# Kernel tuning notes

Hardware: AMD Instinct MI355X
Metric: run time of the kernel (lower is better)

Reference implementation:

```python
import jax, jax.numpy as jnp
import numpy as np
from jax import lax

B, T, IN, H, OUT, OC = 64, 1024, 128, 512, 128, 64


def setup_inputs() -> dict:
    key = jax.random.key(0)
    ks = jax.random.split(key, 9)
    s = 0.05
    return {
        "inX": jax.random.normal(ks[0], (B, T, IN), jnp.float32),
        "r": jnp.zeros((1,), jnp.float32),
        "conv_w": jax.random.normal(ks[1], (OC, IN, 3), jnp.float32) * s,
        "conv_b": jax.random.normal(ks[2], (OC,), jnp.float32) * s,
        "w_ih": jax.random.normal(ks[3], (4 * H, OC), jnp.float32) * s,
        "w_hh": jax.random.normal(ks[4], (4 * H, H), jnp.float32) * s,
        "b_ih": jax.random.normal(ks[5], (4 * H,), jnp.float32) * s,
        "b_hh": jax.random.normal(ks[6], (4 * H,), jnp.float32) * s,
        "lin_w": jax.random.normal(ks[7], (OUT, H), jnp.float32) * s,
        "lin_b": jax.random.normal(ks[8], (OUT,), jnp.float32) * s,
        "batch_size": B,
    }


def reference(inX, r, conv_w, conv_b, w_ih, w_hh, b_ih, b_hh, lin_w, lin_b, batch_size):
    # F.normalize along dim=2 (L2, eps=1e-12)
    nrm = jnp.sqrt(jnp.sum(inX * inX, axis=2, keepdims=True))
    x = inX / jnp.maximum(nrm, 1e-12)
    # [B, C, L] conv1d, valid padding, stride 1
    x = x.transpose(0, 2, 1)
    y = lax.conv_general_dilated(x, conv_w, (1,), "VALID",
                                 dimension_numbers=("NCH", "OIH", "NCH"))
    y = jax.nn.relu(y + conv_b[None, :, None])
    seq = y.transpose(2, 0, 1)  # [T', B, OC]

    h0 = jnp.zeros((batch_size, w_hh.shape[1]), inX.dtype)
    c0 = jnp.zeros_like(h0)

    def step(carry, xt):
        h, c = carry
        gates = xt @ w_ih.T + b_ih + h @ w_hh.T + b_hh
        i, f, g, o = jnp.split(gates, 4, axis=-1)
        c = jax.nn.sigmoid(f) * c + jax.nn.sigmoid(i) * jnp.tanh(g)
        h = jax.nn.sigmoid(o) * jnp.tanh(c)
        return (h, c), None

    (h, c), _ = lax.scan(step, (h0, c0), seq)
    return h @ lin_w.T + lin_b
```

## Files before the change

### kernel.cpp

```cpp
#include <hip/hip_runtime.h>

typedef __attribute__((ext_vector_type(8))) short short8;
typedef __attribute__((ext_vector_type(4))) float f32x4;
typedef unsigned short u16;
typedef unsigned long long u64;

#define TP   1022
#define NWRK 32

#define OFF_WPACK   0
#define OFF_SEQ     2359296
#define OFF_BIAS    10993664
#define OFF_H0      11001856
#define OFF_H1      11067392
#define OFF_HFIN    11132928
#define OFF_BAR     11264000
#define OFF_CWT     11266048

__device__ inline u16 f2bf(float x) {
  union { float f; unsigned u; } un; un.f = x;
  unsigned r = un.u + 0x7fffu + ((un.u >> 16) & 1u);
  return (u16)(r >> 16);
}
__device__ inline float sigmoidf_(float x) { return 1.f / (1.f + __expf(-x)); }
__device__ inline float tanhf_(float x)    { return 2.f / (1.f + __expf(-2.f * x)) - 1.f; }

__device__ inline f32x4 load16_sc0(const void* p) {
  f32x4 r;
  asm volatile("global_load_dwordx4 %0, %1, off sc0" : "=v"(r) : "v"(p) : "memory");
  return r;
}
__device__ inline void store16_sc0(void* p, f32x4 v) {
  asm volatile("global_store_dwordx4 %0, %1, off sc0" :: "v"(p), "v"(v) : "memory");
}

__global__ void k_init(const float* __restrict__ b_ih, const float* __restrict__ b_hh,
                       float* __restrict__ biasp, unsigned* __restrict__ hzero,
                       unsigned* __restrict__ bar) {
  int tid = blockIdx.x * 256 + threadIdx.x;
  if (tid < 32768) hzero[tid] = 0u;
  if (tid < 2048) {
    int j = tid >> 2, g = tid & 3;
    int row = g * 512 + j;
    biasp[tid] = b_ih[row] + b_hh[row];
  }
  if (tid < 128) bar[tid] = 0u;
}

__global__ void k_pack(const float* __restrict__ w_ih, const float* __restrict__ w_hh,
                       u16* __restrict__ wp) {
  int idx = blockIdx.x * 256 + threadIdx.x;
  int nt = idx / 9216;
  int rem = idx - nt * 9216;
  int kt = rem / 512;
  int rem2 = rem - kt * 512;
  int lane = rem2 >> 3, i = rem2 & 7;
  int n = nt * 16 + (lane & 15);
  int k = kt * 32 + (lane >> 4) * 8 + i;
  int j = n >> 2, g = n & 3;
  int row = g * 512 + j;
  float v = (k < 64) ? w_ih[row * 64 + k] : w_hh[row * 512 + (k - 64)];
  wp[idx] = f2bf(v);
}

__global__ void k_packc(const float* __restrict__ conv_w, float* __restrict__ cwT) {
  int idx = blockIdx.x * 256 + threadIdx.x;
  if (idx < 24576) {
    int ik = idx >> 6, oc = idx & 63;
    cwT[ik * 64 + oc] = conv_w[oc * 384 + ik];
  }
}

__global__ __launch_bounds__(256) void k_conv(const float* __restrict__ inX,
                                              const float* __restrict__ cwT,
                                              const float* __restrict__ conv_b,
                                              u16* __restrict__ seq) {
  __shared__ float xn[6][128];
  __shared__ float rn[6];
  int b = blockIdx.y;
  int t0 = blockIdx.x * 4;
  int tid = threadIdx.x;
  for (int e = tid; e < 768; e += 256) {
    int ri = e >> 7, col = e & 127;
    int t = t0 + ri;
    xn[ri][col] = (t < 1024) ? inX[((size_t)b * 1024 + t) * 128 + col] : 0.f;
  }
  __syncthreads();
  if (tid < 192) {
    int ri = tid >> 5, l32 = tid & 31;
    float4 v = *reinterpret_cast<const float4*>(&xn[ri][l32 * 4]);
    float s = v.x * v.x + v.y * v.y + v.z * v.z + v.w * v.w;
    #pragma unroll
    for (int d = 1; d < 32; d <<= 1) s += __shfl_xor(s, d, 32);
    if (l32 == 0) rn[ri] = 1.f / fmaxf(sqrtf(s), 1e-12f);
  }
  __syncthreads();
  for (int e = tid; e < 768; e += 256) {
    int ri = e >> 7, col = e & 127;
    xn[ri][col] *= rn[ri];
  }
  __syncthreads();
  int oc = tid & 63, ty = tid >> 6;
  int t = t0 + ty;
  if (t < TP) {
    const float* wt = cwT + oc;
    float s = conv_b[oc];
    #pragma unroll 8
    for (int i = 0; i < 128; ++i) {
      s += wt[(i * 3 + 0) * 64] * xn[ty + 0][i]
         + wt[(i * 3 + 1) * 64] * xn[ty + 1][i]
         + wt[(i * 3 + 2) * 64] * xn[ty + 2][i];
    }
    s = fmaxf(s, 0.f);
    seq[((size_t)t * 64 + b) * 64 + oc] = f2bf(s);
  }
}

__global__ __launch_bounds__(256, 1) void k_lstm(const u16* __restrict__ seq,
                                                 const u16* __restrict__ wp,
                                                 const float* __restrict__ biasp,
                                                 u16* h0buf, u16* h1buf,
                                                 float* __restrict__ hfin,
                                                 unsigned* bar) {
  const int tid = threadIdx.x;
  __shared__ int s_rank;
  __shared__ __align__(16) char hl[32768];
  __shared__ u16 ostage[32][40];

  if (tid == 0) {
    unsigned xcd;
    asm volatile("s_getreg_b32 %0, hwreg(HW_REG_XCC_ID)" : "=s"(xcd));
    xcd &= 7u;
    unsigned r = __hip_atomic_fetch_add(&bar[8 + xcd], 1u, __ATOMIC_RELAXED,
                                        __HIP_MEMORY_SCOPE_AGENT);
    if (r == NWRK - 1) {
      unsigned expected = 0u;
      __hip_atomic_compare_exchange_strong(&bar[16], &expected, xcd + 1u,
                                           __ATOMIC_RELAXED, __ATOMIC_RELAXED,
                                           __HIP_MEMORY_SCOPE_AGENT);
    }
    unsigned d;
    while ((d = __hip_atomic_load(&bar[16], __ATOMIC_RELAXED,
                                  __HIP_MEMORY_SCOPE_AGENT)) == 0u)
      __builtin_amdgcn_s_sleep(8);
    s_rank = (xcd == d - 1u && r < NWRK) ? (int)r : -1;
  }
  __syncthreads();
  const int rank = s_rank;

  if (rank < 0) {
    const int lane_ = tid & 63;
    float x = (float)tid + 1.0f;
    unsigned d = 0;
    do {
      #pragma unroll
      for (int i = 0; i < 1024; ++i) x = __builtin_fmaf(x, 1.0000001f, 1.0e-30f);
      asm volatile("" :: "v"(x));
      if (lane_ == 0)
        d = __hip_atomic_fetch_add(&bar[96], 0u, __ATOMIC_RELAXED,
                                   __HIP_MEMORY_SCOPE_AGENT);
      d = __shfl(d, 0);
    } while (d < NWRK);
    return;
  }

  const int wave = tid >> 6, lane = tid & 63;
  const int g   = rank >> 4;
  const int wgi = rank & 15;
  const int B0  = g * 32;
  const int U0  = wgi * 32;
  const int mt2 = wgi * 4 + wave;
  const int mtA = 2 * mt2, mtB = mtA + 1;
  const int bl  = lane & 15;
  const int bA  = B0 + bl;
  const int hi  = lane >> 4;
  const int koff = hi * 8;
  const int ulA = 8 * wave + hi;
  const int ulB = ulA + 4;
  const int uA  = U0 + ulA;
  const int uB  = U0 + ulB;
  const float4 biasA = *reinterpret_cast<const float4*>(biasp + mtA * 16 + hi * 4);
  const float4 biasB = *reinterpret_cast<const float4*>(biasp + mtB * 16 + hi * 4);

  short8 wA[18], wB[18];
  {
    const u16* wa = wp + (size_t)mtA * (18 * 512) + lane * 8;
    const u16* wb = wp + (size_t)mtB * (18 * 512) + lane * 8;
    #pragma unroll
    for (int kt = 0; kt < 18; ++kt) {
      wA[kt] = *reinterpret_cast<const short8*>(wa + kt * 512);
      wB[kt] = *reinterpret_cast<const short8*>(wb + kt * 512);
    }
  }

  unsigned* grpcnt = &bar[g * 32];
  float cA0 = 0.f, cA1 = 0.f, cB0 = 0.f, cB1 = 0.f;
  f32x4 accA0, accA1, accB0, accB1;

  const int r0base = bl * 1024;
  const int r1base = r0base + 16 * 1024;
  const int rmask  = (bl & 7) << 4;
  const int fr_hib = hi * 16;

  const int strow = tid >> 5;
  const int stcol = tid & 31;
  const int stswz = strow << 4;

#define XPART(T) do { \
    const u16* xt_ = seq + (size_t)(T) * 4096; \
    short8 x0a = *reinterpret_cast<const short8*>(xt_ + bA * 64 + koff); \
    short8 x1a = *reinterpret_cast<const short8*>(xt_ + (bA + 16) * 64 + koff); \
    short8 x0b = *reinterpret_cast<const short8*>(xt_ + bA * 64 + 32 + koff); \
    short8 x1b = *reinterpret_cast<const short8*>(xt_ + (bA + 16) * 64 + 32 + koff); \
    f32x4 z_ = {0.f, 0.f, 0.f, 0.f}; \
    accA0 = __builtin_amdgcn_mfma_f32_16x16x32_bf16(wA[0], x0a, z_, 0, 0, 0); \
    accA1 = __builtin_amdgcn_mfma_f32_16x16x32_bf16(wA[0], x1a, z_, 0, 0, 0); \
    accB0 = __builtin_amdgcn_mfma_f32_16x16x32_bf16(wB[0], x0a, z_, 0, 0, 0); \
    accB1 = __builtin_amdgcn_mfma_f32_16x16x32_bf16(wB[0], x1a, z_, 0, 0, 0); \
    accA0 = __builtin_amdgcn_mfma_f32_16x16x32_bf16(wA[1], x0b, accA0, 0, 0, 0); \
    accA1 = __builtin_amdgcn_mfma_f32_16x16x32_bf16(wA[1], x1b, accA1, 0, 0, 0); \
    accB0 = __builtin_amdgcn_mfma_f32_16x16x32_bf16(wB[1], x0b, accB0, 0, 0, 0); \
    accB1 = __builtin_amdgcn_mfma_f32_16x16x32_bf16(wB[1], x1b, accB1, 0, 0, 0); \
  } while (0)

  XPART(0);

  for (int t = 0; t < TP; ++t) {
    if (t > 0) {
      if (tid == 0) {
        const unsigned tgt = (unsigned)(16 * t);
        for (;;) {
          unsigned v = __hip_atomic_fetch_add(grpcnt, 0u, __ATOMIC_RELAXED,
                                              __HIP_MEMORY_SCOPE_WORKGROUP);
          if (v >= tgt) break;
          __builtin_amdgcn_s_sleep(1);
        }
      }
      __syncthreads();
    }

    const u16* hc = (t & 1) ? h1buf : h0buf;
    u16* hn = (t & 1) ? h0buf : h1buf;

    const u16* hsrc = hc + (size_t)B0 * 512;
    f32x4 va[4], vb[4];
    #pragma unroll
    for (int p = 0; p < 4; ++p)
      va[p] = load16_sc0(hsrc + (size_t)(p * 8 + strow) * 512 + stcol * 8);
    #pragma unroll
    for (int p = 0; p < 4; ++p)
      vb[p] = load16_sc0(hsrc + (size_t)(p * 8 + strow) * 512 + 256 + stcol * 8);
    asm volatile("s_waitcnt vmcnt(4)" ::: "memory");
    __builtin_amdgcn_sched_barrier(0);
    #pragma unroll
    for (int p = 0; p < 4; ++p)
      *reinterpret_cast<f32x4*>(hl + (p * 8 + strow) * 1024 +
                                ((stcol * 16) ^ stswz)) = va[p];
    __syncthreads();

    #pragma unroll
    for (int kt = 0; kt < 8; ++kt) {
      int off = (kt * 64 + fr_hib) ^ rmask;
      short8 b0 = *reinterpret_cast<const short8*>(hl + r0base + off);
      short8 b1 = *reinterpret_cast<const short8*>(hl + r1base + off);
      accA0 = __builtin_amdgcn_mfma_f32_16x16x32_bf16(wA[kt + 2], b0, accA0, 0, 0, 0);
      accA1 = __builtin_amdgcn_mfma_f32_16x16x32_bf16(wA[kt + 2], b1, accA1, 0, 0, 0);
      accB0 = __builtin_amdgcn_mfma_f32_16x16x32_bf16(wB[kt + 2], b0, accB0, 0, 0, 0);
      accB1 = __builtin_amdgcn_mfma_f32_16x16x32_bf16(wB[kt + 2], b1, accB1, 0, 0, 0);
    }

    asm volatile("s_waitcnt vmcnt(0)" ::: "memory");
    __builtin_amdgcn_sched_barrier(0);
    #pragma unroll
    for (int p = 0; p < 4; ++p)
      *reinterpret_cast<f32x4*>(hl + (p * 8 + strow) * 1024 + 512 +
                                ((stcol * 16) ^ stswz)) = vb[p];
    __syncthreads();
    #pragma unroll
    for (int kt = 8; kt < 16; ++kt) {
      int off = (kt * 64 + fr_hib) ^ rmask;
      short8 b0 = *reinterpret_cast<const short8*>(hl + r0base + off);
      short8 b1 = *reinterpret_cast<const short8*>(hl + r1base + off);
      accA0 = __builtin_amdgcn_mfma_f32_16x16x32_bf16(wA[kt + 2], b0, accA0, 0, 0, 0);
      accA1 = __builtin_amdgcn_mfma_f32_16x16x32_bf16(wA[kt + 2], b1, accA1, 0, 0, 0);
      accB0 = __builtin_amdgcn_mfma_f32_16x16x32_bf16(wB[kt + 2], b0, accB0, 0, 0, 0);
      accB1 = __builtin_amdgcn_mfma_f32_16x16x32_bf16(wB[kt + 2], b1, accB1, 0, 0, 0);
    }

    float iA0 = sigmoidf_(accA0[0] + biasA.x);
    float fA0 = sigmoidf_(accA0[1] + biasA.y);
    float gA0 = tanhf_(accA0[2] + biasA.z);
    float oA0 = sigmoidf_(accA0[3] + biasA.w);
    cA0 = fA0 * cA0 + iA0 * gA0;
    float hvA0 = oA0 * tanhf_(cA0);
    float iA1 = sigmoidf_(accA1[0] + biasA.x);
    float fA1 = sigmoidf_(accA1[1] + biasA.y);
    float gA1 = tanhf_(accA1[2] + biasA.z);
    float oA1 = sigmoidf_(accA1[3] + biasA.w);
    cA1 = fA1 * cA1 + iA1 * gA1;
    float hvA1 = oA1 * tanhf_(cA1);
    float iB0 = sigmoidf_(accB0[0] + biasB.x);
    float fB0 = sigmoidf_(accB0[1] + biasB.y);
    float gB0 = tanhf_(accB0[2] + biasB.z);
    float oB0 = sigmoidf_(accB0[3] + biasB.w);
    cB0 = fB0 * cB0 + iB0 * gB0;
    float hvB0 = oB0 * tanhf_(cB0);
    float iB1 = sigmoidf_(accB1[0] + biasB.x);
    float fB1 = sigmoidf_(accB1[1] + biasB.y);
    float gB1 = tanhf_(accB1[2] + biasB.z);
    float oB1 = sigmoidf_(accB1[3] + biasB.w);
    cB1 = fB1 * cB1 + iB1 * gB1;
    float hvB1 = oB1 * tanhf_(cB1);

    ostage[bl][ulA]      = f2bf(hvA0);
    ostage[bl + 16][ulA] = f2bf(hvA1);
    ostage[bl][ulB]      = f2bf(hvB0);
    ostage[bl + 16][ulB] = f2bf(hvB1);
    if (t == TP - 1) {
      hfin[bA * 512 + uA]        = hvA0;
      hfin[(bA + 16) * 512 + uA] = hvA1;
      hfin[bA * 512 + uB]        = hvB0;
      hfin[(bA + 16) * 512 + uB] = hvB1;
    }
    __syncthreads();

    if (tid < 128) {
      int b_l = tid >> 2, q = tid & 3;
      f32x4 val = *reinterpret_cast<const f32x4*>(&ostage[b_l][q * 8]);
      store16_sc0(hn + (size_t)(B0 + b_l) * 512 + U0 + q * 8, val);
    }
    asm volatile("s_waitcnt vmcnt(0)" ::: "memory");
    __syncthreads();

    if (tid == 0)
      __hip_atomic_fetch_add(grpcnt, 1u, __ATOMIC_RELAXED, __HIP_MEMORY_SCOPE_WORKGROUP);

    if (t + 1 < TP) XPART(t + 1);
  }
#undef XPART

  if (tid == 0)
    __hip_atomic_fetch_add(&bar[96], 1u, __ATOMIC_RELAXED, __HIP_MEMORY_SCOPE_AGENT);
}

__global__ void k_fc(const float* __restrict__ hfin, const float* __restrict__ lin_w,
                     const float* __restrict__ lin_b, float* __restrict__ out) {
  int b = blockIdx.x, o = threadIdx.x;
  const float4* hp = reinterpret_cast<const float4*>(hfin + b * 512);
  const float4* wq = reinterpret_cast<const float4*>(lin_w + o * 512);
  float s = lin_b[o];
  #pragma unroll 8
  for (int j = 0; j < 128; ++j) {
    float4 h4 = hp[j], w4 = wq[j];
    s += h4.x * w4.x + h4.y * w4.y + h4.z * w4.z + h4.w * w4.w;
  }
  out[b * 128 + o] = s;
}

extern "C" void kernel_launch(void* const* d_in, const int* in_sizes, int n_in,
                              void* d_out, int out_size, void* d_ws, size_t ws_size,
                              hipStream_t stream) {
  const float* inX    = (const float*)d_in[0];
  const float* conv_w = (const float*)d_in[2];
  const float* conv_b = (const float*)d_in[3];
  const float* w_ih   = (const float*)d_in[4];
  const float* w_hh   = (const float*)d_in[5];
  const float* b_ih   = (const float*)d_in[6];
  const float* b_hh   = (const float*)d_in[7];
  const float* lin_w  = (const float*)d_in[8];
  const float* lin_b  = (const float*)d_in[9];
  float* out = (float*)d_out;
  char* ws = (char*)d_ws;
  u16*      wpack = (u16*)(ws + OFF_WPACK);
  u16*      seq   = (u16*)(ws + OFF_SEQ);
  float*    biasp = (float*)(ws + OFF_BIAS);
  u16*      h0b   = (u16*)(ws + OFF_H0);
  u16*      h1b   = (u16*)(ws + OFF_H1);
  float*    hfin  = (float*)(ws + OFF_HFIN);
  unsigned* bar   = (unsigned*)(ws + OFF_BAR);
  float*    cwT   = (float*)(ws + OFF_CWT);

  k_init<<<dim3(128), dim3(256), 0, stream>>>(b_ih, b_hh, biasp, (unsigned*)(ws + OFF_H0), bar);
  k_pack<<<dim3(4608), dim3(256), 0, stream>>>(w_ih, w_hh, wpack);
  k_packc<<<dim3(96), dim3(256), 0, stream>>>(conv_w, cwT);
  k_conv<<<dim3(256, 64), dim3(256), 0, stream>>>(inX, cwT, conv_b, seq);
  k_lstm<<<dim3(256), dim3(256), 0, stream>>>(seq, wpack, biasp, h0b, h1b, hfin, bar);
  k_fc<<<dim3(64), dim3(128), 0, stream>>>(hfin, lin_w, lin_b, out);
}
```

Measured before the change: 3.459 ms.

## Restructure conv kernel for register tiling and fold weight transpose into init

The conv kernel now gives each block one batch item and a quarter of its timesteps, processed in 64-step chunks. Input rows go into swizzled shared memory, and each thread accumulates 16 output channels in registers with wave-uniform weight loads. Normalisation is applied on the fly, and results are staged in shared memory for coalesced bf16 stores. The conv-weight transpose moves into the init kernel, removing one launch. The grid shrinks to 256 blocks with heavy shared memory use, so there is less parallelism than the old 16K-block grid, and the LSTM kernel still dominates total time.

Result: faster. 3.322 ms (-4.0%).

```diff
diff --git a/kernel.cpp b/kernel.cpp
--- a/kernel.cpp
+++ b/kernel.cpp
@@ -35,8 +35,9 @@
 }
 
 __global__ void k_init(const float* __restrict__ b_ih, const float* __restrict__ b_hh,
+                       const float* __restrict__ conv_w,
                        float* __restrict__ biasp, unsigned* __restrict__ hzero,
-                       unsigned* __restrict__ bar) {
+                       unsigned* __restrict__ bar, float* __restrict__ cwT) {
   int tid = blockIdx.x * 256 + threadIdx.x;
   if (tid < 32768) hzero[tid] = 0u;
   if (tid < 2048) {
@@ -45,6 +46,10 @@
     biasp[tid] = b_ih[row] + b_hh[row];
   }
   if (tid < 128) bar[tid] = 0u;
+  if (tid < 24576) {
+    int ik = tid >> 6, oc = tid & 63;
+    cwT[ik * 64 + oc] = conv_w[oc * 384 + ik];
+  }
 }
 
 __global__ void k_pack(const float* __restrict__ w_ih, const float* __restrict__ w_hh,
@@ -63,56 +68,82 @@
   wp[idx] = f2bf(v);
 }
 
-__global__ void k_packc(const float* __restrict__ conv_w, float* __restrict__ cwT) {
-  int idx = blockIdx.x * 256 + threadIdx.x;
-  if (idx < 24576) {
-    int ik = idx >> 6, oc = idx & 63;
-    cwT[ik * 64 + oc] = conv_w[oc * 384 + ik];
-  }
-}
-
 __global__ __launch_bounds__(256) void k_conv(const float* __restrict__ inX,
                                               const float* __restrict__ cwT,
                                               const float* __restrict__ conv_b,
                                               u16* __restrict__ seq) {
-  __shared__ float xn[6][128];
-  __shared__ float rn[6];
-  int b = blockIdx.y;
-  int t0 = blockIdx.x * 4;
-  int tid = threadIdx.x;
-  for (int e = tid; e < 768; e += 256) {
-    int ri = e >> 7, col = e & 127;
-    int t = t0 + ri;
-    xn[ri][col] = (t < 1024) ? inX[((size_t)b * 1024 + t) * 128 + col] : 0.f;
-  }
-  __syncthreads();
-  if (tid < 192) {
-    int ri = tid >> 5, l32 = tid & 31;
-    float4 v = *reinterpret_cast<const float4*>(&xn[ri][l32 * 4]);
-    float s = v.x * v.x + v.y * v.y + v.z * v.z + v.w * v.w;
-    #pragma unroll
-    for (int d = 1; d < 32; d <<= 1) s += __shfl_xor(s, d, 32);
-    if (l32 == 0) rn[ri] = 1.f / fmaxf(sqrtf(s), 1e-12f);
-  }
-  __syncthreads();
-  for (int e = tid; e < 768; e += 256) {
-    int ri = e >> 7, col = e & 127;
-    xn[ri][col] *= rn[ri];
-  }
-  __syncthreads();
-  int oc = tid & 63, ty = tid >> 6;
-  int t = t0 + ty;
-  if (t < TP) {
-    const float* wt = cwT + oc;
-    float s = conv_b[oc];
-    #pragma unroll 8
-    for (int i = 0; i < 128; ++i) {
-      s += wt[(i * 3 + 0) * 64] * xn[ty + 0][i]
-         + wt[(i * 3 + 1) * 64] * xn[ty + 1][i]
-         + wt[(i * 3 + 2) * 64] * xn[ty + 2][i];
-    }
-    s = fmaxf(s, 0.f);
-    seq[((size_t)t * 64 + b) * 64 + oc] = f2bf(s);
+  __shared__ float xs[66 * 128];
+  __shared__ float rn[66];
+  __shared__ u16 outb[64 * 64];
+  const int tid = threadIdx.x;
+  const int b = blockIdx.x >> 2;
+  const int q = blockIdx.x & 3;
+  const int wave = tid >> 6;
+  const int oc0 = __builtin_amdgcn_readfirstlane(wave * 16);
+  const int tl = tid & 63;
+  const float4 bias4a = *reinterpret_cast<const float4*>(conv_b + oc0);
+  const float4 bias4b = *reinterpret_cast<const float4*>(conv_b + oc0 + 4);
+  const float4 bias4c = *reinterpret_cast<const float4*>(conv_b + oc0 + 8);
+  const float4 bias4d = *reinterpret_cast<const float4*>(conv_b + oc0 + 12);
+
+  for (int c = 0; c < 4; ++c) {
+    const int t0 = (q * 4 + c) * 64;
+    for (int e = tid; e < 66 * 128; e += 256) {
+      int tt = e >> 7, i = e & 127;
+      int gt = t0 + tt;
+      float v = (gt < 1024) ? inX[((size_t)b * 1024 + gt) * 128 + i] : 0.f;
+      xs[tt * 128 + (i ^ (tt & 31))] = v;
+    }
+    __syncthreads();
+    {
+      int g32 = tid >> 5, l32 = tid & 31;
+      for (int r = g32; r < 66; r += 8) {
+        float s = 0.f;
+        #pragma unroll
+        for (int jj = 0; jj < 4; ++jj) {
+          float v = xs[r * 128 + ((l32 * 4 + jj) ^ (r & 31))];
+          s += v * v;
+        }
+        #pragma unroll
+        for (int d = 1; d < 32; d <<= 1) s += __shfl_xor(s, d, 32);
+        if (l32 == 0) rn[r] = 1.f / fmaxf(sqrtf(s), 1e-12f);
+      }
+    }
+    __syncthreads();
+    {
+      float acc[16];
+      #pragma unroll
+      for (int j = 0; j < 16; ++j) acc[j] = 0.f;
+      const float rn0 = rn[tl], rn1 = rn[tl + 1], rn2 = rn[tl + 2];
+      const int a0 = (tl + 0) * 128, m0 = (tl + 0) & 31;
+      const int a1 = (tl + 1) * 128, m1 = (tl + 1) & 31;
+      const int a2 = (tl + 2) * 128, m2 = (tl + 2) & 31;
+      for (int i = 0; i < 128; ++i) {
+        float x0 = xs[a0 + (i ^ m0)] * rn0;
+        float x1 = xs[a1 + (i ^ m1)] * rn1;
+        float x2 = xs[a2 + (i ^ m2)] * rn2;
+        const float* w0 = cwT + (i * 3 + 0) * 64 + oc0;
+        const float* w1 = cwT + (i * 3 + 1) * 64 + oc0;
+        const float* w2 = cwT + (i * 3 + 2) * 64 + oc0;
+        #pragma unroll
+        for (int j = 0; j < 16; ++j)
+          acc[j] += w0[j] * x0 + w1[j] * x1 + w2[j] * x2;
+      }
+      const float bj[16] = {bias4a.x, bias4a.y, bias4a.z, bias4a.w,
+                            bias4b.x, bias4b.y, bias4b.z, bias4b.w,
+                            bias4c.x, bias4c.y, bias4c.z, bias4c.w,
+                            bias4d.x, bias4d.y, bias4d.z, bias4d.w};
+      #pragma unroll
+      for (int j = 0; j < 16; ++j)
+        outb[tl * 64 + oc0 + j] = f2bf(fmaxf(acc[j] + bj[j], 0.f));
+    }
+    __syncthreads();
+    for (int e = tid; e < 4096; e += 256) {
+      int tt = e >> 6, oc = e & 63;
+      int gt = t0 + tt;
+      if (gt < TP) seq[((size_t)gt * 64 + b) * 64 + oc] = outb[tt * 64 + oc];
+    }
+    __syncthreads();
   }
 }
 
@@ -380,10 +411,10 @@
   unsigned* bar   = (unsigned*)(ws + OFF_BAR);
   float*    cwT   = (float*)(ws + OFF_CWT);
 
-  k_init<<<dim3(128), dim3(256), 0, stream>>>(b_ih, b_hh, biasp, (unsigned*)(ws + OFF_H0), bar);
+  k_init<<<dim3(128), dim3(256), 0, stream>>>(b_ih, b_hh, conv_w, biasp,
+                                              (unsigned*)(ws + OFF_H0), bar, cwT);
   k_pack<<<dim3(4608), dim3(256), 0, stream>>>(w_ih, w_hh, wpack);
-  k_packc<<<dim3(96), dim3(256), 0, stream>>>(conv_w, cwT);
-  k_conv<<<dim3(256, 64), dim3(256), 0, stream>>>(inX, cwT, conv_b, seq);
+  k_conv<<<dim3(256), dim3(256), 0, stream>>>(inX, cwT, conv_b, seq);
   k_lstm<<<dim3(256), dim3(256), 0, stream>>>(seq, wpack, biasp, h0b, h1b, hfin, bar);
   k_fc<<<dim3(64), dim3(128), 0, stream>>>(hfin, lin_w, lin_b, out);
 }
```
